# Optimization experiments

Hardware: AMD Instinct MI355X
Metric: run time of the kernel (lower is better)

The kernel has to match this reference:

```python
import jax, jax.numpy as jnp
import numpy as np
from jax import lax

WS = 11
SIGMA = 1.5
C1 = 0.01 ** 2
C2 = 0.03 ** 2


def _gauss_kernel(size=WS, sigma=SIGMA):
    c = jnp.arange(size, dtype=jnp.float32) - size // 2
    g = jnp.exp(-c ** 2 / (2 * sigma ** 2))
    g = g / g.sum()
    k = g[None, :] * g[:, None]              # (ws, ws)
    return k[None, None, :, :]               # (O=1, I=1, ws, ws)


def _depthwise_conv(x, k, C):
    pad = WS // 2
    kC = jnp.broadcast_to(k, (C, 1, WS, WS))  # groups=C depthwise
    return lax.conv_general_dilated(
        x, kC, window_strides=(1, 1), padding=[(pad, pad), (pad, pad)],
        dimension_numbers=('NCHW', 'OIHW', 'NCHW'), feature_group_count=C)


def _ssim_pair(pred, target, k):
    pred = (pred + 1.0) / 2.0
    target = (target + 1.0) / 2.0
    C = pred.shape[1]
    mu1 = _depthwise_conv(pred, k, C)
    mu2 = _depthwise_conv(target, k, C)
    mu1_sq = mu1 * mu1
    mu2_sq = mu2 * mu2
    mu12 = mu1 * mu2
    s1 = _depthwise_conv(pred * pred, k, C) - mu1_sq
    s2 = _depthwise_conv(target * target, k, C) - mu2_sq
    s12 = _depthwise_conv(pred * target, k, C) - mu12
    num = (2.0 * mu12 + C1) * (2.0 * s12 + C2)
    den = (mu1_sq + mu2_sq + C1) * (s1 + s2 + C2)
    return jnp.mean(num / den)


def setup_inputs() -> dict:
    key = jax.random.key(0)
    k1, k2, k3 = jax.random.split(key, 3)
    shape = (16, 1, 512, 512)
    # images in [-1, 1]
    fused = jax.random.uniform(k1, shape, jnp.float32, -1.0, 1.0)
    img_a = jax.random.uniform(k2, shape, jnp.float32, -1.0, 1.0)
    img_b = jax.random.uniform(k3, shape, jnp.float32, -1.0, 1.0)
    return {"fused": fused, "img_a": img_a, "img_b": img_b}


def reference(fused, img_a, img_b):
    k = _gauss_kernel()
    ssim_a = _ssim_pair(fused, img_a, k)
    ssim_b = _ssim_pair(fused, img_b, k)
    return 1.0 - (ssim_a + ssim_b) / 2.0
```

## Files before the change

kernel.cpp:

```cpp
#include <hip/hip_runtime.h>

#define NT 256
#define TW 32
#define TH 16
#define IH (TH + 10)
#define HP 33
#define IMW 512
#define IMH 512
#define NSLOT 64
#define SLOTSTRIDE 16

typedef float f32x2 __attribute__((ext_vector_type(2)));

__device__ __forceinline__ float wave_reduce(float v) {
    #pragma unroll
    for (int off = 32; off > 0; off >>= 1)
        v += __shfl_down(v, off, 64);
    return v;
}

__device__ __forceinline__ int swz(int i) { return i ^ (i >> 3); }

#define G0 0.00102838f
#define G1 0.00759840f
#define G2 0.03600077f
#define G3 0.10936070f
#define G4 0.21300590f
#define G5 0.26601190f

template<bool BORDER>
__device__ __forceinline__ void h_pass(
    const float* __restrict__ Fp, const float* __restrict__ Ap,
    const float* __restrict__ Bp, int x0, int y0, int tid,
    float4* __restrict__ h4a, float4* __restrict__ h4b)
{
    const float g[11] = {G0, G1, G2, G3, G4, G5, G4, G3, G2, G1, G0};
    if (tid >= IH * 8) return;
    const int r  = tid >> 3;
    const int cg = tid & 7;
    const int gy = y0 + r - 5;
    bool yok = true;
    if (BORDER) yok = (gy >= 0) && (gy < IMH);

    f32x2 accs[4][4];
    #pragma unroll
    for (int k = 0; k < 4; ++k)
        #pragma unroll
        for (int q = 0; q < 4; ++q) accs[k][q] = (f32x2){0.f, 0.f};

    const int xbase = x0 + 4 * cg - 8;
    #pragma unroll
    for (int w = 0; w < 5; ++w) {
        const int xc = xbase + 4 * w;
        float4 p4 = {-1.f, -1.f, -1.f, -1.f};
        float4 a4 = {-1.f, -1.f, -1.f, -1.f};
        float4 b4 = {-1.f, -1.f, -1.f, -1.f};
        bool ld = true;
        if (BORDER) ld = yok && (xc >= 0) && (xc < IMW);
        if (ld) {
            const size_t o = ((size_t)gy * IMW + xc) >> 2;
            p4 = ((const float4*)Fp)[o];
            a4 = ((const float4*)Ap)[o];
            b4 = ((const float4*)Bp)[o];
        }
        const float pe[4] = {p4.x, p4.y, p4.z, p4.w};
        const float ae[4] = {a4.x, a4.y, a4.z, a4.w};
        const float be[4] = {b4.x, b4.y, b4.z, b4.w};
        #pragma unroll
        for (int e = 0; e < 4; ++e) {
            const int i = 4 * w + e;
            if (i < 3 || i >= 17) continue;
            const int t = i - 3;
            const float p = fmaf(pe[e], 0.5f, 0.5f);
            const float a = fmaf(ae[e], 0.5f, 0.5f);
            const float b = fmaf(be[e], 0.5f, 0.5f);
            const f32x2 v_pa   = {p, a};
            const f32x2 v_ab   = {a, b};
            const f32x2 v_pp2  = {p, p};
            const f32x2 v_ppaa = v_pa * v_pa;
            const f32x2 v_papb = v_pp2 * v_ab;
            const f32x2 v_bbb  = {b, b * b};
            #pragma unroll
            for (int k = 0; k < 4; ++k) {
                const int j = t - k;
                if (j < 0 || j > 10) continue;
                const f32x2 w2 = {g[j], g[j]};
                accs[k][0] += w2 * v_pa;
                accs[k][1] += w2 * v_bbb;
                accs[k][2] += w2 * v_ppaa;
                accs[k][3] += w2 * v_papb;
            }
        }
    }
    #pragma unroll
    for (int k = 0; k < 4; ++k) {
        const int sc = swz(4 * cg + k);
        h4a[r * HP + sc] = make_float4(accs[k][0].x, accs[k][0].y,
                                       accs[k][1].x, accs[k][1].y);
        h4b[r * HP + sc] = make_float4(accs[k][2].x, accs[k][2].y,
                                       accs[k][3].x, accs[k][3].y);
    }
}

__global__ __launch_bounds__(NT, 5) void ssim_main_kernel(
    const float* __restrict__ fused,
    const float* __restrict__ img_a,
    const float* __restrict__ img_b,
    float* __restrict__ acc_slots)
{
    __shared__ float4 h4a[IH * HP];
    __shared__ float4 h4b[IH * HP];
    __shared__ float red[NT / 64];

    const float g[11] = {G0, G1, G2, G3, G4, G5, G4, G3, G2, G1, G0};

    const int tid = threadIdx.x;
    const int x0 = blockIdx.x * TW;
    const int y0 = blockIdx.y * TH;
    const size_t ioff = (size_t)blockIdx.z * IMW * IMH;
    const float* Fp = fused + ioff;
    const float* Ap = img_a + ioff;
    const float* Bp = img_b + ioff;

    const bool border = (blockIdx.x == 0) | (blockIdx.x == gridDim.x - 1) |
                        (blockIdx.y == 0) | (blockIdx.y == gridDim.y - 1);
    if (border) h_pass<true >(Fp, Ap, Bp, x0, y0, tid, h4a, h4b);
    else        h_pass<false>(Fp, Ap, Bp, x0, y0, tid, h4a, h4b);
    __syncthreads();

    const float C1v = 1e-4f;
    const float C2v = 9e-4f;
    float lsum = 0.f;
    {
        const int c  = tid & 31;
        const int rg = tid >> 5;
        const int R0 = rg * 2;
        const int sc = swz(c);

        f32x2 m2[2][4];
        #pragma unroll
        for (int k = 0; k < 2; ++k)
            #pragma unroll
            for (int q = 0; q < 4; ++q) m2[k][q] = (f32x2){0.f, 0.f};

        #pragma unroll
        for (int j = 0; j < 12; ++j) {
            const float4 va = h4a[(R0 + j) * HP + sc];
            const float4 vb = h4b[(R0 + j) * HP + sc];
            const f32x2 va01 = {va.x, va.y};
            const f32x2 va23 = {va.z, va.w};
            const f32x2 vb01 = {vb.x, vb.y};
            const f32x2 vb23 = {vb.z, vb.w};
            #pragma unroll
            for (int k = 0; k < 2; ++k) {
                const int t = j - k;
                if (t < 0 || t > 10) continue;
                const f32x2 w2 = {g[t], g[t]};
                m2[k][0] += w2 * va01;
                m2[k][1] += w2 * va23;
                m2[k][2] += w2 * vb01;
                m2[k][3] += w2 * vb23;
            }
        }
        #pragma unroll
        for (int k = 0; k < 2; ++k) {
            const float mp  = m2[k][0].x, ma  = m2[k][0].y;
            const float mb  = m2[k][1].x, mbb = m2[k][1].y;
            const float mpp = m2[k][2].x, maa = m2[k][2].y;
            const float mpa = m2[k][3].x, mpb = m2[k][3].y;
            const float mp2 = mp * mp, ma2 = ma * ma, mb2 = mb * mb;
            const float s_p  = mpp - mp2;
            const float s_a  = maa - ma2;
            const float s_b  = mbb - mb2;
            const float s_pa = mpa - mp * ma;
            const float s_pb = mpb - mp * mb;
            const float na = (2.f * mp * ma + C1v) * (2.f * s_pa + C2v);
            const float da = (mp2 + ma2 + C1v) * (s_p + s_a + C2v);
            const float nb = (2.f * mp * mb + C1v) * (2.f * s_pb + C2v);
            const float db = (mp2 + mb2 + C1v) * (s_p + s_b + C2v);
            lsum += na * __builtin_amdgcn_rcpf(da)
                  + nb * __builtin_amdgcn_rcpf(db);
        }
    }

    lsum = wave_reduce(lsum);
    if ((tid & 63) == 0) red[tid >> 6] = lsum;
    __syncthreads();
    if (tid == 0) {
        float s = 0.f;
        #pragma unroll
        for (int i = 0; i < NT / 64; ++i) s += red[i];
        const int lin = blockIdx.x + (int)gridDim.x * (blockIdx.y + (int)gridDim.y * blockIdx.z);
        atomicAdd(&acc_slots[(lin & (NSLOT - 1)) * SLOTSTRIDE], s);
    }
}

__global__ void ssim_finalize_kernel(const float* __restrict__ acc_slots,
                                     float* __restrict__ out, float invTwoN) {
    float v = acc_slots[threadIdx.x * SLOTSTRIDE];
    v = wave_reduce(v);
    if (threadIdx.x == 0) out[0] = 1.f - v * invTwoN;
}

extern "C" void kernel_launch(void* const* d_in, const int* in_sizes, int n_in,
                              void* d_out, int out_size, void* d_ws, size_t ws_size,
                              hipStream_t stream) {
    const float* fused = (const float*)d_in[0];
    const float* img_a = (const float*)d_in[1];
    const float* img_b = (const float*)d_in[2];
    float* out = (float*)d_out;
    float* acc = (float*)d_ws;

    hipMemsetAsync(acc, 0, NSLOT * SLOTSTRIDE * sizeof(float), stream);

    dim3 grid(IMW / TW, IMH / TH, 16);
    ssim_main_kernel<<<grid, NT, 0, stream>>>(fused, img_a, img_b, acc);

    const float invTwoN = 1.f / (2.f * 16.f * (float)IMW * (float)IMH);
    ssim_finalize_kernel<<<1, 64, 0, stream>>>(acc, out, invTwoN);
}
```

Before: 119.0 us.

## Replace atomic slot accumulation with per-block partials and drop memset

Each block now writes its partial sum to its own slot instead of doing an atomicAdd into one of 64 strided slots. This removes the hipMemsetAsync launch and the atomic contention. A wider finalize kernel reads all 8192 partials with float4 loads. The change also sets the LDS row pitch HP from 33 to 32 (the xor swizzle still spreads banks) and raises the launch_bounds occupancy hint from 5 to 6, trading some register headroom for more resident blocks.

```diff
diff --git a/kernel.cpp b/kernel.cpp
--- a/kernel.cpp
+++ b/kernel.cpp
@@ -4,11 +4,10 @@
 #define TW 32
 #define TH 16
 #define IH (TH + 10)
-#define HP 33
+#define HP 32
 #define IMW 512
 #define IMH 512
-#define NSLOT 64
-#define SLOTSTRIDE 16
+#define NBLK ((IMW / TW) * (IMH / TH) * 16)
 
 typedef float f32x2 __attribute__((ext_vector_type(2)));
 
@@ -102,11 +101,11 @@
     }
 }
 
-__global__ __launch_bounds__(NT, 5) void ssim_main_kernel(
+__global__ __launch_bounds__(NT, 6) void ssim_main_kernel(
     const float* __restrict__ fused,
     const float* __restrict__ img_a,
     const float* __restrict__ img_b,
-    float* __restrict__ acc_slots)
+    float* __restrict__ slots)
 {
     __shared__ float4 h4a[IH * HP];
     __shared__ float4 h4b[IH * HP];
@@ -187,19 +186,26 @@
     if ((tid & 63) == 0) red[tid >> 6] = lsum;
     __syncthreads();
     if (tid == 0) {
-        float s = 0.f;
-        #pragma unroll
-        for (int i = 0; i < NT / 64; ++i) s += red[i];
         const int lin = blockIdx.x + (int)gridDim.x * (blockIdx.y + (int)gridDim.y * blockIdx.z);
-        atomicAdd(&acc_slots[(lin & (NSLOT - 1)) * SLOTSTRIDE], s);
-    }
-}
-
-__global__ void ssim_finalize_kernel(const float* __restrict__ acc_slots,
-                                     float* __restrict__ out, float invTwoN) {
-    float v = acc_slots[threadIdx.x * SLOTSTRIDE];
-    v = wave_reduce(v);
-    if (threadIdx.x == 0) out[0] = 1.f - v * invTwoN;
+        slots[lin] = red[0] + red[1] + red[2] + red[3];
+    }
+}
+
+__global__ __launch_bounds__(NT) void ssim_finalize_kernel(
+    const float* __restrict__ slots, float* __restrict__ out, float invTwoN)
+{
+    __shared__ float red[NT / 64];
+    float s = 0.f;
+    const float4* s4 = (const float4*)slots;
+    for (int i = threadIdx.x; i < NBLK / 4; i += NT) {
+        const float4 v = s4[i];
+        s += (v.x + v.y) + (v.z + v.w);
+    }
+    s = wave_reduce(s);
+    if ((threadIdx.x & 63) == 0) red[threadIdx.x >> 6] = s;
+    __syncthreads();
+    if (threadIdx.x == 0)
+        out[0] = 1.f - (red[0] + red[1] + red[2] + red[3]) * invTwoN;
 }
 
 extern "C" void kernel_launch(void* const* d_in, const int* in_sizes, int n_in,
@@ -209,13 +215,11 @@
     const float* img_a = (const float*)d_in[1];
     const float* img_b = (const float*)d_in[2];
     float* out = (float*)d_out;
-    float* acc = (float*)d_ws;
-
-    hipMemsetAsync(acc, 0, NSLOT * SLOTSTRIDE * sizeof(float), stream);
+    float* slots = (float*)d_ws;
 
     dim3 grid(IMW / TW, IMH / TH, 16);
-    ssim_main_kernel<<<grid, NT, 0, stream>>>(fused, img_a, img_b, acc);
+    ssim_main_kernel<<<grid, NT, 0, stream>>>(fused, img_a, img_b, slots);
 
     const float invTwoN = 1.f / (2.f * 16.f * (float)IMW * (float)IMH);
-    ssim_finalize_kernel<<<1, 64, 0, stream>>>(acc, out, invTwoN);
-}
+    ssim_finalize_kernel<<<1, NT, 0, stream>>>(slots, out, invTwoN);
+}
```

Result: no change. 118.9 us (-0.1%).
